# Kernel optimization log

Measured on AMD Instinct MI355X. Metric: run time of the kernel, lower is better.

The kernel has to match this reference:

```python
import jax, jax.numpy as jnp
import numpy as np

N = [80000, 70000, 50000]   # entities per type (flattened over the ragged batch)
F = [64, 128, 48]           # feature width per entity type
D = 512                     # d_model
B = 64                      # number of episodes in the ragged batch
EPS_IN = 1e-4               # InputNorm eps
EPS_LN = 1e-5               # LayerNorm eps
CLIP = 5.0                  # InputNorm cliprange


def setup_inputs() -> dict:
    key = jax.random.key(0)
    ks = jax.random.split(key, 3 * 7 + 2)
    inp = {}
    for i, (n, f) in enumerate(zip(N, F)):
        base = 7 * i
        inp[f"ent{i}"] = jax.random.normal(ks[base], (n, f), dtype=jnp.float32)
        inp[f"mean{i}"] = 0.1 * jax.random.normal(ks[base + 1], (f,), dtype=jnp.float32)
        inp[f"var{i}"] = jax.random.uniform(ks[base + 2], (f,), minval=0.5, maxval=1.5, dtype=jnp.float32)
        inp[f"W{i}"] = jax.random.normal(ks[base + 3], (f, D), dtype=jnp.float32) / np.sqrt(f)
        inp[f"b{i}"] = jnp.zeros((D,), dtype=jnp.float32)
        inp[f"gamma{i}"] = jnp.ones((D,), dtype=jnp.float32)
        inp[f"beta{i}"] = jnp.zeros((D,), dtype=jnp.float32)
    total = sum(N)
    # index_map: permutation reassembling per-type blocks into ragged episode order
    inp["index_map"] = jax.random.permutation(ks[-2], total).astype(jnp.int64)
    inp["batch_index"] = jnp.sort(jax.random.randint(ks[-1], (total,), 0, B)).astype(jnp.int64)
    return inp


def _embed(x, mean, var, W, b, gamma, beta):
    # InputNorm: normalize with running stats, clip outliers
    h = jnp.clip((x - mean) * jax.lax.rsqrt(var + EPS_IN), -CLIP, CLIP)
    # Linear + ReLU
    h = jnp.maximum(h @ W + b, 0.0)
    # LayerNorm
    mu = h.mean(-1, keepdims=True)
    v = ((h - mu) ** 2).mean(-1, keepdims=True)
    return gamma * (h - mu) * jax.lax.rsqrt(v + EPS_LN) + beta


def reference(ent0, mean0, var0, W0, b0, gamma0, beta0,
              ent1, mean1, var1, W1, b1, gamma1, beta1,
              ent2, mean2, var2, W2, b2, gamma2, beta2,
              index_map, batch_index):
    embeds = [
        _embed(ent0, mean0, var0, W0, b0, gamma0, beta0),
        _embed(ent1, mean1, var1, W1, b1, gamma1, beta1),
        _embed(ent2, mean2, var2, W2, b2, gamma2, beta2),
    ]
    x = jnp.concatenate(embeds, axis=0)                      # [sum(N), D]
    entity_type = jnp.concatenate(
        [jnp.full((n, 1), float(i), dtype=jnp.float32) for i, n in enumerate(N)], axis=0
    )
    # ragged reorder: gather-based reassembly into episode-major order
    x = x[index_map]
    entity_types = entity_type[index_map]
    tbatch_index = batch_index[index_map]
    return x, tbatch_index, entity_types
```

## Files before the change

kernel.cpp:

```cpp
#include <hip/hip_runtime.h>

#define DMODEL 512
#define EPS_IN 1e-4f
#define EPS_LN 1e-5f
#define CLIPV  5.0f

typedef float f32x4 __attribute__((ext_vector_type(4)));
typedef short s16x8 __attribute__((ext_vector_type(8)));

__device__ __forceinline__ unsigned short f2bf(float f) {
    union { float f; unsigned u; } v; v.f = f;
    unsigned r = v.u + 0x7fffu + ((v.u >> 16) & 1u);
    return (unsigned short)(r >> 16);
}

struct TypeParams {
    const float* x;
    const float* ss;
    const unsigned short* Wt;
    const float* b; const float* gamma; const float* beta;
    int n;
    int offset;
    int nb;
};

__global__ __launch_bounds__(256) void setup_all(
    const int* __restrict__ index_map, const int* __restrict__ batch_index,
    int* __restrict__ inv, float* __restrict__ out_t, float* __restrict__ out_e,
    int total, int n0, int n01, int nbA,
    const float* __restrict__ W0, const float* __restrict__ W1, const float* __restrict__ W2,
    unsigned short* __restrict__ Wt0, unsigned short* __restrict__ Wt1, unsigned short* __restrict__ Wt2,
    const float* __restrict__ mean0, const float* __restrict__ var0,
    const float* __restrict__ mean1, const float* __restrict__ var1,
    const float* __restrict__ mean2, const float* __restrict__ var2,
    float* __restrict__ ss0, float* __restrict__ ss1, float* __restrict__ ss2)
{
    const int nbB = (DMODEL * 256) / 256;
    if (blockIdx.x < (unsigned)nbA) {
        const int j = blockIdx.x * 256 + threadIdx.x;
        if (j >= total) return;
        const int r = index_map[j];
        inv[r] = j;
        out_t[j] = (float)batch_index[r];
        out_e[j] = (r < n0) ? 0.0f : ((r < n01) ? 1.0f : 2.0f);
    } else if (blockIdx.x < (unsigned)(nbA + nbB)) {
        int idx = (blockIdx.x - nbA) * 256 + threadIdx.x;
        const float* W; unsigned short* Wt; int K, Kp;
        if (idx < DMODEL * 64)              { W = W0; Wt = Wt0; K = 64;  Kp = 64; }
        else if (idx < DMODEL * (64 + 128)) { idx -= DMODEL * 64;  W = W1; Wt = Wt1; K = 128; Kp = 128; }
        else                                { idx -= DMODEL * 192; W = W2; Wt = Wt2; K = 48;  Kp = 64; }
        const int nn = idx / Kp, k = idx - nn * Kp;
        const float w = (k < K) ? W[(size_t)k * DMODEL + nn] : 0.0f;
        Wt[idx] = f2bf(w);
    } else {
        const int c = threadIdx.x;
        if (c < 64)  { const float s = rsqrtf(var0[c] + EPS_IN); ss0[c] = s; ss0[64 + c]  = -mean0[c] * s; }
        if (c < 128) { const float s = rsqrtf(var1[c] + EPS_IN); ss1[c] = s; ss1[128 + c] = -mean1[c] * s; }
        if (c < 48)  { const float s = rsqrtf(var2[c] + EPS_IN); ss2[c] = s; ss2[48 + c]  = -mean2[c] * s; }
    }
}

template<int F, int KP>
__device__ __forceinline__ void embed_body(
    const TypeParams& p, int bid, const int* __restrict__ inv,
    float* __restrict__ out, char* lds)
{
    const int tid  = threadIdx.x;
    const int lane = tid & 63;
    const int wn   = tid >> 6;
    const int l15  = lane & 15;
    const int g    = lane >> 4;
    const int row0 = bid * 32;
    const int n    = p.n;
    constexpr int SEG = KP / 8;
    constexpr int NKS = KP / 32;

    float2* red = reinterpret_cast<float2*>(lds + NKS * 2048);

    if (tid < 32 * SEG) {
        const int r = tid & 31;
        const int s = tid >> 5;
        const int gr = row0 + r;
        const int c = s * 8;
        s16x8 pk;
#pragma unroll
        for (int jj = 0; jj < 8; ++jj) pk[jj] = 0;
        if (gr < n && c < F) {
            const float4 x0 = *(const float4*)(p.x + (size_t)gr * F + c);
            const float4 x1 = *(const float4*)(p.x + (size_t)gr * F + c + 4);
            const float4 sc0 = *(const float4*)(p.ss + c);
            const float4 sc1 = *(const float4*)(p.ss + c + 4);
            const float4 sh0 = *(const float4*)(p.ss + F + c);
            const float4 sh1 = *(const float4*)(p.ss + F + c + 4);
            float t[8];
            t[0] = fmaf(x0.x, sc0.x, sh0.x); t[1] = fmaf(x0.y, sc0.y, sh0.y);
            t[2] = fmaf(x0.z, sc0.z, sh0.z); t[3] = fmaf(x0.w, sc0.w, sh0.w);
            t[4] = fmaf(x1.x, sc1.x, sh1.x); t[5] = fmaf(x1.y, sc1.y, sh1.y);
            t[6] = fmaf(x1.z, sc1.z, sh1.z); t[7] = fmaf(x1.w, sc1.w, sh1.w);
#pragma unroll
            for (int jj = 0; jj < 8; ++jj)
                pk[jj] = (short)f2bf(fminf(fmaxf(t[jj], -CLIPV), CLIPV));
        }
        *reinterpret_cast<s16x8*>(lds + tid * 16) = pk;
    }
    __syncthreads();

    int orow[2];
#pragma unroll
    for (int m = 0; m < 2; ++m) {
        const int rg = row0 + m * 16 + l15;
        orow[m] = (rg < n) ? inv[p.offset + rg] : -1;
    }

    f32x4 acc[2][4];
#pragma unroll
    for (int m = 0; m < 2; ++m)
#pragma unroll
        for (int t = 0; t < 4; ++t) acc[m][t] = (f32x4)0.0f;

    const unsigned short* wtl = p.Wt + (size_t)(wn * 64 + l15) * KP + g * 8;

#pragma unroll
    for (int ks = 0; ks < NKS; ++ks) {
        const int ab = ((ks * 4 + g) * 32 + l15) * 16;
        const s16x8 a0 = *reinterpret_cast<const s16x8*>(lds + ab);
        const s16x8 a1 = *reinterpret_cast<const s16x8*>(lds + ab + 256);
#pragma unroll
        for (int t = 0; t < 4; ++t) {
            const s16x8 wf = *reinterpret_cast<const s16x8*>(wtl + (size_t)t * 16 * KP + ks * 32);
            acc[0][t] = __builtin_amdgcn_mfma_f32_16x16x32_bf16(wf, a0, acc[0][t], 0, 0, 0);
            acc[1][t] = __builtin_amdgcn_mfma_f32_16x16x32_bf16(wf, a1, acc[1][t], 0, 0, 0);
        }
    }

#pragma unroll
    for (int t = 0; t < 4; ++t) {
        const float4 bb = *(const float4*)(p.b + wn * 64 + t * 16 + g * 4);
#pragma unroll
        for (int m = 0; m < 2; ++m) {
            acc[m][t][0] = fmaxf(acc[m][t][0] + bb.x, 0.0f);
            acc[m][t][1] = fmaxf(acc[m][t][1] + bb.y, 0.0f);
            acc[m][t][2] = fmaxf(acc[m][t][2] + bb.z, 0.0f);
            acc[m][t][3] = fmaxf(acc[m][t][3] + bb.w, 0.0f);
        }
    }

    {
        float ps[2] = {0.0f, 0.0f}, pq[2] = {0.0f, 0.0f};
#pragma unroll
        for (int m = 0; m < 2; ++m)
#pragma unroll
            for (int t = 0; t < 4; ++t)
#pragma unroll
                for (int j = 0; j < 4; ++j) {
                    const float v = acc[m][t][j];
                    ps[m] += v;
                    pq[m] = fmaf(v, v, pq[m]);
                }
#pragma unroll
        for (int m = 0; m < 2; ++m) {
            ps[m] += __shfl_xor(ps[m], 16, 64);
            pq[m] += __shfl_xor(pq[m], 16, 64);
            ps[m] += __shfl_xor(ps[m], 32, 64);
            pq[m] += __shfl_xor(pq[m], 32, 64);
        }
        if (g == 0) {
#pragma unroll
            for (int m = 0; m < 2; ++m)
                red[(m * 16 + l15) * 8 + wn] = make_float2(ps[m], pq[m]);
        }
    }
    __syncthreads();

#pragma unroll
    for (int m = 0; m < 2; ++m) {
        const int od = orow[m];
        if (od < 0) continue;
        const int rl = m * 16 + l15;
        float s = 0.0f, q = 0.0f;
#pragma unroll
        for (int wq = 0; wq < 8; ++wq) { const float2 e = red[rl * 8 + wq]; s += e.x; q += e.y; }
        const float mu = s * (1.0f / DMODEL);
        const float vv = fmaxf(q * (1.0f / DMODEL) - mu * mu, 0.0f);
        const float sc = rsqrtf(vv + EPS_LN);
        float* op = out + (size_t)od * DMODEL + wn * 64 + g * 4;
#pragma unroll
        for (int t = 0; t < 4; ++t) {
            const float4 gg = *(const float4*)(p.gamma + wn * 64 + t * 16 + g * 4);
            const float4 ee = *(const float4*)(p.beta  + wn * 64 + t * 16 + g * 4);
            float4 o;
            o.x = fmaf(gg.x * sc, acc[m][t][0] - mu, ee.x);
            o.y = fmaf(gg.y * sc, acc[m][t][1] - mu, ee.y);
            o.z = fmaf(gg.z * sc, acc[m][t][2] - mu, ee.z);
            o.w = fmaf(gg.w * sc, acc[m][t][3] - mu, ee.w);
            *(float4*)(op + t * 16) = o;
        }
    }
}

__global__ __launch_bounds__(512, 6) void embed_all(
    TypeParams p0, TypeParams p1, TypeParams p2,
    const int* __restrict__ inv, float* __restrict__ out)
{
    extern __shared__ char lds[];
    const int bid = blockIdx.x;
    if (bid < p0.nb)                embed_body<64, 64>  (p0, bid, inv, out, lds);
    else if (bid < p0.nb + p1.nb)   embed_body<128, 128>(p1, bid - p0.nb, inv, out, lds);
    else                            embed_body<48, 64>  (p2, bid - p0.nb - p1.nb, inv, out, lds);
}

extern "C" void kernel_launch(void* const* d_in, const int* in_sizes, int n_in,
                              void* d_out, int out_size, void* d_ws, size_t ws_size,
                              hipStream_t stream)
{
    const int F0 = 64, F1 = 128, F2 = 48;
    const int n0 = in_sizes[0]  / F0;
    const int n1 = in_sizes[7]  / F1;
    const int n2 = in_sizes[14] / F2;
    const int total = n0 + n1 + n2;

    float* out   = (float*)d_out;
    float* out_t = out + (size_t)total * DMODEL;
    float* out_e = out_t + total;

    int* inv = (int*)d_ws;
    unsigned short* Wt0 = (unsigned short*)((char*)d_ws + (((size_t)total * 4 + 255) & ~(size_t)255));
    unsigned short* Wt1 = Wt0 + DMODEL * 64;
    unsigned short* Wt2 = Wt1 + DMODEL * 128;
    float* ss0 = (float*)(Wt2 + DMODEL * 64);
    float* ss1 = ss0 + 128;
    float* ss2 = ss1 + 256;

    const int* index_map   = (const int*)d_in[21];
    const int* batch_index = (const int*)d_in[22];

    const int nbA = (total + 255) / 256;
    const int nbB = (DMODEL * 256) / 256;
    setup_all<<<nbA + nbB + 1, 256, 0, stream>>>(
        index_map, batch_index, inv, out_t, out_e, total, n0, n0 + n1, nbA,
        (const float*)d_in[3], (const float*)d_in[10], (const float*)d_in[17],
        Wt0, Wt1, Wt2,
        (const float*)d_in[1],  (const float*)d_in[2],
        (const float*)d_in[8],  (const float*)d_in[9],
        (const float*)d_in[15], (const float*)d_in[16],
        ss0, ss1, ss2);

    TypeParams p0{(const float*)d_in[0],  ss0, Wt0,
                  (const float*)d_in[4],  (const float*)d_in[5],  (const float*)d_in[6],
                  n0, 0,       (n0 + 31) / 32};
    TypeParams p1{(const float*)d_in[7],  ss1, Wt1,
                  (const float*)d_in[11], (const float*)d_in[12], (const float*)d_in[13],
                  n1, n0,      (n1 + 31) / 32};
    TypeParams p2{(const float*)d_in[14], ss2, Wt2,
                  (const float*)d_in[18], (const float*)d_in[19], (const float*)d_in[20],
                  n2, n0 + n1, (n2 + 31) / 32};

    const int nb = p0.nb + p1.nb + p2.nb;
    const int lds_size = 4 * 2048 + 32 * 8 * sizeof(float2);
    embed_all<<<nb, 512, lds_size, stream>>>(p0, p1, p2, inv, out);
}
```

Measured before the change: 185.8 us.

## Make embed blocks persistent over tiles with double-buffered prefetch of next tile

Each block now processes about four 32-row tiles in a strided loop instead of one. The next tile's input rows and inverse indices are loaded into registers during the current tile's MFMA and LayerNorm work, and staging alternates between two LDS buffers. Per-type scale/shift vectors are hoisted out of the loop. This adds registers and LDS per block and lowers the occupancy hint from 6 to 4 waves, with fewer blocks to spread across CUs.

```diff
diff --git a/kernel.cpp b/kernel.cpp
--- a/kernel.cpp
+++ b/kernel.cpp
@@ -65,140 +65,177 @@
     const TypeParams& p, int bid, const int* __restrict__ inv,
     float* __restrict__ out, char* lds)
 {
+    constexpr int SEG    = KP / 8;
+    constexpr int ABYTES = 32 * KP * 2;
+    constexpr int NKS    = KP / 32;
     const int tid  = threadIdx.x;
     const int lane = tid & 63;
     const int wn   = tid >> 6;
     const int l15  = lane & 15;
     const int g    = lane >> 4;
-    const int row0 = bid * 32;
     const int n    = p.n;
-    constexpr int SEG = KP / 8;
-    constexpr int NKS = KP / 32;
-
-    float2* red = reinterpret_cast<float2*>(lds + NKS * 2048);
-
-    if (tid < 32 * SEG) {
-        const int r = tid & 31;
-        const int s = tid >> 5;
-        const int gr = row0 + r;
-        const int c = s * 8;
+    const int NB   = p.nb;
+    const int ntiles = (n + 31) >> 5;
+
+    float2* red = reinterpret_cast<float2*>(lds + 2 * ABYTES);
+
+    const bool stg  = tid < 32 * SEG;
+    const int  sr   = tid & 31;
+    const int  scol = (tid >> 5) * 8;
+
+    float4 sA0 = {0,0,0,0}, sA1 = {0,0,0,0}, sB0 = {0,0,0,0}, sB1 = {0,0,0,0};
+    if (stg && scol < F) {
+        sA0 = *(const float4*)(p.ss + scol);
+        sA1 = *(const float4*)(p.ss + scol + 4);
+        sB0 = *(const float4*)(p.ss + F + scol);
+        sB1 = *(const float4*)(p.ss + F + scol + 4);
+    }
+
+    auto loadx = [&](int t, float4& x0, float4& x1) {
+        x0 = float4{0,0,0,0}; x1 = x0;
+        const int row = t * 32 + sr;
+        if (stg && row < n && scol < F) {
+            x0 = *(const float4*)(p.x + (size_t)row * F + scol);
+            x1 = *(const float4*)(p.x + (size_t)row * F + scol + 4);
+        }
+    };
+    auto loadinv = [&](int t, int* o) {
+#pragma unroll
+        for (int m = 0; m < 2; ++m) {
+            const int rg = t * 32 + m * 16 + l15;
+            o[m] = (rg < n) ? inv[p.offset + rg] : -1;
+        }
+    };
+    auto transform = [&](const float4& x0, const float4& x1) -> s16x8 {
+        float tv[8];
+        tv[0] = fmaf(x0.x, sA0.x, sB0.x); tv[1] = fmaf(x0.y, sA0.y, sB0.y);
+        tv[2] = fmaf(x0.z, sA0.z, sB0.z); tv[3] = fmaf(x0.w, sA0.w, sB0.w);
+        tv[4] = fmaf(x1.x, sA1.x, sB1.x); tv[5] = fmaf(x1.y, sA1.y, sB1.y);
+        tv[6] = fmaf(x1.z, sA1.z, sB1.z); tv[7] = fmaf(x1.w, sA1.w, sB1.w);
         s16x8 pk;
 #pragma unroll
-        for (int jj = 0; jj < 8; ++jj) pk[jj] = 0;
-        if (gr < n && c < F) {
-            const float4 x0 = *(const float4*)(p.x + (size_t)gr * F + c);
-            const float4 x1 = *(const float4*)(p.x + (size_t)gr * F + c + 4);
-            const float4 sc0 = *(const float4*)(p.ss + c);
-            const float4 sc1 = *(const float4*)(p.ss + c + 4);
-            const float4 sh0 = *(const float4*)(p.ss + F + c);
-            const float4 sh1 = *(const float4*)(p.ss + F + c + 4);
-            float t[8];
-            t[0] = fmaf(x0.x, sc0.x, sh0.x); t[1] = fmaf(x0.y, sc0.y, sh0.y);
-            t[2] = fmaf(x0.z, sc0.z, sh0.z); t[3] = fmaf(x0.w, sc0.w, sh0.w);
-            t[4] = fmaf(x1.x, sc1.x, sh1.x); t[5] = fmaf(x1.y, sc1.y, sh1.y);
-            t[6] = fmaf(x1.z, sc1.z, sh1.z); t[7] = fmaf(x1.w, sc1.w, sh1.w);
-#pragma unroll
-            for (int jj = 0; jj < 8; ++jj)
-                pk[jj] = (short)f2bf(fminf(fmaxf(t[jj], -CLIPV), CLIPV));
-        }
-        *reinterpret_cast<s16x8*>(lds + tid * 16) = pk;
+        for (int jj = 0; jj < 8; ++jj)
+            pk[jj] = (short)f2bf(fminf(fmaxf(tv[jj], -CLIPV), CLIPV));
+        return pk;
+    };
+
+    int tile = bid;
+    if (tile >= ntiles) return;
+    s16x8 pk;
+    int corow[2];
+    {
+        float4 x0, x1;
+        loadx(tile, x0, x1);
+        loadinv(tile, corow);
+        pk = transform(x0, x1);
     }
-    __syncthreads();
-
-    int orow[2];
-#pragma unroll
-    for (int m = 0; m < 2; ++m) {
-        const int rg = row0 + m * 16 + l15;
-        orow[m] = (rg < n) ? inv[p.offset + rg] : -1;
+    int pipe = 0;
+
+    const unsigned short* wtl = p.Wt + (size_t)(wn * 64 + l15) * KP + g * 8;
+
+    while (tile < ntiles) {
+        const int next = tile + NB;
+        const bool hn = next < ntiles;
+
+        if (stg) *reinterpret_cast<s16x8*>(lds + pipe * ABYTES + tid * 16) = pk;
+        __syncthreads();
+
+        float4 nx0 = {0,0,0,0}, nx1 = {0,0,0,0};
+        int norow[2] = {-1, -1};
+        if (hn) { loadx(next, nx0, nx1); loadinv(next, norow); }
+
+        f32x4 acc[2][4];
+#pragma unroll
+        for (int m = 0; m < 2; ++m)
+#pragma unroll
+            for (int t = 0; t < 4; ++t) acc[m][t] = (f32x4)0.0f;
+
+        const char* ab = lds + pipe * ABYTES;
+#pragma unroll
+        for (int ks = 0; ks < NKS; ++ks) {
+            const int off = ((ks * 4 + g) * 32 + l15) * 16;
+            const s16x8 a0 = *reinterpret_cast<const s16x8*>(ab + off);
+            const s16x8 a1 = *reinterpret_cast<const s16x8*>(ab + off + 256);
+#pragma unroll
+            for (int t = 0; t < 4; ++t) {
+                const s16x8 wf = *reinterpret_cast<const s16x8*>(wtl + (size_t)t * 16 * KP + ks * 32);
+                acc[0][t] = __builtin_amdgcn_mfma_f32_16x16x32_bf16(wf, a0, acc[0][t], 0, 0, 0);
+                acc[1][t] = __builtin_amdgcn_mfma_f32_16x16x32_bf16(wf, a1, acc[1][t], 0, 0, 0);
+            }
+        }
+
+#pragma unroll
+        for (int t = 0; t < 4; ++t) {
+            const float4 bb = *(const float4*)(p.b + wn * 64 + t * 16 + g * 4);
+#pragma unroll
+            for (int m = 0; m < 2; ++m) {
+                acc[m][t][0] = fmaxf(acc[m][t][0] + bb.x, 0.0f);
+                acc[m][t][1] = fmaxf(acc[m][t][1] + bb.y, 0.0f);
+                acc[m][t][2] = fmaxf(acc[m][t][2] + bb.z, 0.0f);
+                acc[m][t][3] = fmaxf(acc[m][t][3] + bb.w, 0.0f);
+            }
+        }
+
+        {
+            float ps[2] = {0.0f, 0.0f}, pq[2] = {0.0f, 0.0f};
+#pragma unroll
+            for (int m = 0; m < 2; ++m)
+#pragma unroll
+                for (int t = 0; t < 4; ++t)
+#pragma unroll
+                    for (int j = 0; j < 4; ++j) {
+                        const float v = acc[m][t][j];
+                        ps[m] += v;
+                        pq[m] = fmaf(v, v, pq[m]);
+                    }
+#pragma unroll
+            for (int m = 0; m < 2; ++m) {
+                ps[m] += __shfl_xor(ps[m], 16, 64);
+                pq[m] += __shfl_xor(pq[m], 16, 64);
+                ps[m] += __shfl_xor(ps[m], 32, 64);
+                pq[m] += __shfl_xor(pq[m], 32, 64);
+            }
+            if (g == 0) {
+#pragma unroll
+                for (int m = 0; m < 2; ++m)
+                    red[(m * 16 + l15) * 8 + wn] = make_float2(ps[m], pq[m]);
+            }
+        }
+        __syncthreads();
+
+#pragma unroll
+        for (int m = 0; m < 2; ++m) {
+            const int od = corow[m];
+            if (od < 0) continue;
+            const int rl = m * 16 + l15;
+            float s = 0.0f, q = 0.0f;
+#pragma unroll
+            for (int wq = 0; wq < 8; ++wq) { const float2 e = red[rl * 8 + wq]; s += e.x; q += e.y; }
+            const float mu = s * (1.0f / DMODEL);
+            const float vv = fmaxf(q * (1.0f / DMODEL) - mu * mu, 0.0f);
+            const float sc = rsqrtf(vv + EPS_LN);
+            float* op = out + (size_t)od * DMODEL + wn * 64 + g * 4;
+#pragma unroll
+            for (int t = 0; t < 4; ++t) {
+                const float4 gg = *(const float4*)(p.gamma + wn * 64 + t * 16 + g * 4);
+                const float4 ee = *(const float4*)(p.beta  + wn * 64 + t * 16 + g * 4);
+                float4 o;
+                o.x = fmaf(gg.x * sc, acc[m][t][0] - mu, ee.x);
+                o.y = fmaf(gg.y * sc, acc[m][t][1] - mu, ee.y);
+                o.z = fmaf(gg.z * sc, acc[m][t][2] - mu, ee.z);
+                o.w = fmaf(gg.w * sc, acc[m][t][3] - mu, ee.w);
+                *(float4*)(op + t * 16) = o;
+            }
+        }
+
+        pk = transform(nx0, nx1);
+        corow[0] = norow[0]; corow[1] = norow[1];
+        pipe ^= 1;
+        tile = next;
     }
-
-    f32x4 acc[2][4];
-#pragma unroll
-    for (int m = 0; m < 2; ++m)
-#pragma unroll
-        for (int t = 0; t < 4; ++t) acc[m][t] = (f32x4)0.0f;
-
-    const unsigned short* wtl = p.Wt + (size_t)(wn * 64 + l15) * KP + g * 8;
-
-#pragma unroll
-    for (int ks = 0; ks < NKS; ++ks) {
-        const int ab = ((ks * 4 + g) * 32 + l15) * 16;
-        const s16x8 a0 = *reinterpret_cast<const s16x8*>(lds + ab);
-        const s16x8 a1 = *reinterpret_cast<const s16x8*>(lds + ab + 256);
-#pragma unroll
-        for (int t = 0; t < 4; ++t) {
-            const s16x8 wf = *reinterpret_cast<const s16x8*>(wtl + (size_t)t * 16 * KP + ks * 32);
-            acc[0][t] = __builtin_amdgcn_mfma_f32_16x16x32_bf16(wf, a0, acc[0][t], 0, 0, 0);
-            acc[1][t] = __builtin_amdgcn_mfma_f32_16x16x32_bf16(wf, a1, acc[1][t], 0, 0, 0);
-        }
-    }
-
-#pragma unroll
-    for (int t = 0; t < 4; ++t) {
-        const float4 bb = *(const float4*)(p.b + wn * 64 + t * 16 + g * 4);
-#pragma unroll
-        for (int m = 0; m < 2; ++m) {
-            acc[m][t][0] = fmaxf(acc[m][t][0] + bb.x, 0.0f);
-            acc[m][t][1] = fmaxf(acc[m][t][1] + bb.y, 0.0f);
-            acc[m][t][2] = fmaxf(acc[m][t][2] + bb.z, 0.0f);
-            acc[m][t][3] = fmaxf(acc[m][t][3] + bb.w, 0.0f);
-        }
-    }
-
-    {
-        float ps[2] = {0.0f, 0.0f}, pq[2] = {0.0f, 0.0f};
-#pragma unroll
-        for (int m = 0; m < 2; ++m)
-#pragma unroll
-            for (int t = 0; t < 4; ++t)
-#pragma unroll
-                for (int j = 0; j < 4; ++j) {
-                    const float v = acc[m][t][j];
-                    ps[m] += v;
-                    pq[m] = fmaf(v, v, pq[m]);
-                }
-#pragma unroll
-        for (int m = 0; m < 2; ++m) {
-            ps[m] += __shfl_xor(ps[m], 16, 64);
-            pq[m] += __shfl_xor(pq[m], 16, 64);
-            ps[m] += __shfl_xor(ps[m], 32, 64);
-            pq[m] += __shfl_xor(pq[m], 32, 64);
-        }
-        if (g == 0) {
-#pragma unroll
-            for (int m = 0; m < 2; ++m)
-                red[(m * 16 + l15) * 8 + wn] = make_float2(ps[m], pq[m]);
-        }
-    }
-    __syncthreads();
-
-#pragma unroll
-    for (int m = 0; m < 2; ++m) {
-        const int od = orow[m];
-        if (od < 0) continue;
-        const int rl = m * 16 + l15;
-        float s = 0.0f, q = 0.0f;
-#pragma unroll
-        for (int wq = 0; wq < 8; ++wq) { const float2 e = red[rl * 8 + wq]; s += e.x; q += e.y; }
-        const float mu = s * (1.0f / DMODEL);
-        const float vv = fmaxf(q * (1.0f / DMODEL) - mu * mu, 0.0f);
-        const float sc = rsqrtf(vv + EPS_LN);
-        float* op = out + (size_t)od * DMODEL + wn * 64 + g * 4;
-#pragma unroll
-        for (int t = 0; t < 4; ++t) {
-            const float4 gg = *(const float4*)(p.gamma + wn * 64 + t * 16 + g * 4);
-            const float4 ee = *(const float4*)(p.beta  + wn * 64 + t * 16 + g * 4);
-            float4 o;
-            o.x = fmaf(gg.x * sc, acc[m][t][0] - mu, ee.x);
-            o.y = fmaf(gg.y * sc, acc[m][t][1] - mu, ee.y);
-            o.z = fmaf(gg.z * sc, acc[m][t][2] - mu, ee.z);
-            o.w = fmaf(gg.w * sc, acc[m][t][3] - mu, ee.w);
-            *(float4*)(op + t * 16) = o;
-        }
-    }
-}
-
-__global__ __launch_bounds__(512, 6) void embed_all(
+}
+
+__global__ __launch_bounds__(512, 4) void embed_all(
     TypeParams p0, TypeParams p1, TypeParams p2,
     const int* __restrict__ inv, float* __restrict__ out)
 {
@@ -218,6 +255,7 @@
     const int n1 = in_sizes[7]  / F1;
     const int n2 = in_sizes[14] / F2;
     const int total = n0 + n1 + n2;
+    const int TPB = 4;
 
     float* out   = (float*)d_out;
     float* out_t = out + (size_t)total * DMODEL;
@@ -245,17 +283,22 @@
         (const float*)d_in[15], (const float*)d_in[16],
         ss0, ss1, ss2);
 
+    const int nt0 = (n0 + 31) / 32, nt1 = (n1 + 31) / 32, nt2 = (n2 + 31) / 32;
+    const int NB0 = (nt0 + TPB - 1) / TPB;
+    const int NB1 = (nt1 + TPB - 1) / TPB;
+    const int NB2 = (nt2 + TPB - 1) / TPB;
+
     TypeParams p0{(const float*)d_in[0],  ss0, Wt0,
                   (const float*)d_in[4],  (const float*)d_in[5],  (const float*)d_in[6],
-                  n0, 0,       (n0 + 31) / 32};
+                  n0, 0,       NB0};
     TypeParams p1{(const float*)d_in[7],  ss1, Wt1,
                   (const float*)d_in[11], (const float*)d_in[12], (const float*)d_in[13],
-                  n1, n0,      (n1 + 31) / 32};
+                  n1, n0,      NB1};
     TypeParams p2{(const float*)d_in[14], ss2, Wt2,
                   (const float*)d_in[18], (const float*)d_in[19], (const float*)d_in[20],
-                  n2, n0 + n1, (n2 + 31) / 32};
-
-    const int nb = p0.nb + p1.nb + p2.nb;
-    const int lds_size = 4 * 2048 + 32 * 8 * sizeof(float2);
+                  n2, n0 + n1, NB2};
+
+    const int nb = NB0 + NB1 + NB2;
+    const int lds_size = 2 * (32 * 128 * 2) + 32 * 8 * sizeof(float2);
     embed_all<<<nb, 512, lds_size, stream>>>(p0, p1, p2, inv, out);
 }
```

New measurement: 218.7 us. 17.7% more time.

## Retile embed kernel to 16-row tiles with 4 waves covering 128 columns each

Applied to the files above, without the earlier changes.

Each block now handles 16 rows with 256 threads, and each wave computes 128 output columns (8 MFMA tiles) instead of 32 rows with 8 waves of 64 columns. This shrinks LDS use and the cross-wave LayerNorm reduction and doubles the block count. In exchange, each loaded weight fragment is reused for only one A tile instead of two, so weight traffic per row rises, and the launch bounds change to 256 threads with 5 blocks per CU.

```diff
diff --git a/kernel.cpp b/kernel.cpp
--- a/kernel.cpp
+++ b/kernel.cpp
@@ -62,36 +62,35 @@
 
 template<int F, int KP>
 __device__ __forceinline__ void embed_body(
-    const TypeParams& p, int bid, const int* __restrict__ inv,
+    const TypeParams& p, int tile, const int* __restrict__ inv,
     float* __restrict__ out, char* lds)
 {
+    constexpr int SEG = KP / 8;
+    constexpr int NKS = KP / 32;
     const int tid  = threadIdx.x;
     const int lane = tid & 63;
     const int wn   = tid >> 6;
     const int l15  = lane & 15;
     const int g    = lane >> 4;
-    const int row0 = bid * 32;
+    const int row0 = tile * 16;
     const int n    = p.n;
-    constexpr int SEG = KP / 8;
-    constexpr int NKS = KP / 32;
-
-    float2* red = reinterpret_cast<float2*>(lds + NKS * 2048);
-
-    if (tid < 32 * SEG) {
-        const int r = tid & 31;
-        const int s = tid >> 5;
+
+    float2* red = reinterpret_cast<float2*>(lds + 16 * KP * 2);
+
+    if (tid < 16 * SEG) {
+        const int r = tid & 15;
+        const int scol = (tid >> 4) * 8;
         const int gr = row0 + r;
-        const int c = s * 8;
         s16x8 pk;
 #pragma unroll
         for (int jj = 0; jj < 8; ++jj) pk[jj] = 0;
-        if (gr < n && c < F) {
-            const float4 x0 = *(const float4*)(p.x + (size_t)gr * F + c);
-            const float4 x1 = *(const float4*)(p.x + (size_t)gr * F + c + 4);
-            const float4 sc0 = *(const float4*)(p.ss + c);
-            const float4 sc1 = *(const float4*)(p.ss + c + 4);
-            const float4 sh0 = *(const float4*)(p.ss + F + c);
-            const float4 sh1 = *(const float4*)(p.ss + F + c + 4);
+        if (gr < n && scol < F) {
+            const float4 x0 = *(const float4*)(p.x + (size_t)gr * F + scol);
+            const float4 x1 = *(const float4*)(p.x + (size_t)gr * F + scol + 4);
+            const float4 sc0 = *(const float4*)(p.ss + scol);
+            const float4 sc1 = *(const float4*)(p.ss + scol + 4);
+            const float4 sh0 = *(const float4*)(p.ss + F + scol);
+            const float4 sh1 = *(const float4*)(p.ss + F + scol + 4);
             float t[8];
             t[0] = fmaf(x0.x, sc0.x, sh0.x); t[1] = fmaf(x0.y, sc0.y, sh0.y);
             t[2] = fmaf(x0.z, sc0.z, sh0.z); t[3] = fmaf(x0.w, sc0.w, sh0.w);
@@ -105,100 +104,75 @@
     }
     __syncthreads();
 
-    int orow[2];
-#pragma unroll
-    for (int m = 0; m < 2; ++m) {
-        const int rg = row0 + m * 16 + l15;
-        orow[m] = (rg < n) ? inv[p.offset + rg] : -1;
-    }
-
-    f32x4 acc[2][4];
-#pragma unroll
-    for (int m = 0; m < 2; ++m)
-#pragma unroll
-        for (int t = 0; t < 4; ++t) acc[m][t] = (f32x4)0.0f;
-
-    const unsigned short* wtl = p.Wt + (size_t)(wn * 64 + l15) * KP + g * 8;
+    const int rg = row0 + l15;
+    const int od = (rg < n) ? inv[p.offset + rg] : -1;
+
+    f32x4 acc[8];
+#pragma unroll
+    for (int t = 0; t < 8; ++t) acc[t] = (f32x4)0.0f;
+
+    const unsigned short* wtl = p.Wt + (size_t)(wn * 128 + l15) * KP + g * 8;
 
 #pragma unroll
     for (int ks = 0; ks < NKS; ++ks) {
-        const int ab = ((ks * 4 + g) * 32 + l15) * 16;
-        const s16x8 a0 = *reinterpret_cast<const s16x8*>(lds + ab);
-        const s16x8 a1 = *reinterpret_cast<const s16x8*>(lds + ab + 256);
-#pragma unroll
-        for (int t = 0; t < 4; ++t) {
+        const s16x8 a = *reinterpret_cast<const s16x8*>(lds + (ks * 4 + g) * 256 + l15 * 16);
+#pragma unroll
+        for (int t = 0; t < 8; ++t) {
             const s16x8 wf = *reinterpret_cast<const s16x8*>(wtl + (size_t)t * 16 * KP + ks * 32);
-            acc[0][t] = __builtin_amdgcn_mfma_f32_16x16x32_bf16(wf, a0, acc[0][t], 0, 0, 0);
-            acc[1][t] = __builtin_amdgcn_mfma_f32_16x16x32_bf16(wf, a1, acc[1][t], 0, 0, 0);
+            acc[t] = __builtin_amdgcn_mfma_f32_16x16x32_bf16(wf, a, acc[t], 0, 0, 0);
         }
     }
 
 #pragma unroll
-    for (int t = 0; t < 4; ++t) {
-        const float4 bb = *(const float4*)(p.b + wn * 64 + t * 16 + g * 4);
-#pragma unroll
-        for (int m = 0; m < 2; ++m) {
-            acc[m][t][0] = fmaxf(acc[m][t][0] + bb.x, 0.0f);
-            acc[m][t][1] = fmaxf(acc[m][t][1] + bb.y, 0.0f);
-            acc[m][t][2] = fmaxf(acc[m][t][2] + bb.z, 0.0f);
-            acc[m][t][3] = fmaxf(acc[m][t][3] + bb.w, 0.0f);
-        }
+    for (int t = 0; t < 8; ++t) {
+        const float4 bb = *(const float4*)(p.b + wn * 128 + t * 16 + g * 4);
+        acc[t][0] = fmaxf(acc[t][0] + bb.x, 0.0f);
+        acc[t][1] = fmaxf(acc[t][1] + bb.y, 0.0f);
+        acc[t][2] = fmaxf(acc[t][2] + bb.z, 0.0f);
+        acc[t][3] = fmaxf(acc[t][3] + bb.w, 0.0f);
     }
 
     {
-        float ps[2] = {0.0f, 0.0f}, pq[2] = {0.0f, 0.0f};
-#pragma unroll
-        for (int m = 0; m < 2; ++m)
-#pragma unroll
-            for (int t = 0; t < 4; ++t)
-#pragma unroll
-                for (int j = 0; j < 4; ++j) {
-                    const float v = acc[m][t][j];
-                    ps[m] += v;
-                    pq[m] = fmaf(v, v, pq[m]);
-                }
-#pragma unroll
-        for (int m = 0; m < 2; ++m) {
-            ps[m] += __shfl_xor(ps[m], 16, 64);
-            pq[m] += __shfl_xor(pq[m], 16, 64);
-            ps[m] += __shfl_xor(ps[m], 32, 64);
-            pq[m] += __shfl_xor(pq[m], 32, 64);
-        }
-        if (g == 0) {
-#pragma unroll
-            for (int m = 0; m < 2; ++m)
-                red[(m * 16 + l15) * 8 + wn] = make_float2(ps[m], pq[m]);
-        }
+        float ps = 0.0f, pq = 0.0f;
+#pragma unroll
+        for (int t = 0; t < 8; ++t)
+#pragma unroll
+            for (int j = 0; j < 4; ++j) {
+                const float v = acc[t][j];
+                ps += v;
+                pq = fmaf(v, v, pq);
+            }
+        ps += __shfl_xor(ps, 16, 64);
+        pq += __shfl_xor(pq, 16, 64);
+        ps += __shfl_xor(ps, 32, 64);
+        pq += __shfl_xor(pq, 32, 64);
+        if (g == 0) red[l15 * 4 + wn] = make_float2(ps, pq);
     }
     __syncthreads();
 
-#pragma unroll
-    for (int m = 0; m < 2; ++m) {
-        const int od = orow[m];
-        if (od < 0) continue;
-        const int rl = m * 16 + l15;
+    if (od >= 0) {
         float s = 0.0f, q = 0.0f;
 #pragma unroll
-        for (int wq = 0; wq < 8; ++wq) { const float2 e = red[rl * 8 + wq]; s += e.x; q += e.y; }
+        for (int wq = 0; wq < 4; ++wq) { const float2 e = red[l15 * 4 + wq]; s += e.x; q += e.y; }
         const float mu = s * (1.0f / DMODEL);
         const float vv = fmaxf(q * (1.0f / DMODEL) - mu * mu, 0.0f);
         const float sc = rsqrtf(vv + EPS_LN);
-        float* op = out + (size_t)od * DMODEL + wn * 64 + g * 4;
-#pragma unroll
-        for (int t = 0; t < 4; ++t) {
-            const float4 gg = *(const float4*)(p.gamma + wn * 64 + t * 16 + g * 4);
-            const float4 ee = *(const float4*)(p.beta  + wn * 64 + t * 16 + g * 4);
+        float* op = out + (size_t)od * DMODEL + wn * 128 + g * 4;
+#pragma unroll
+        for (int t = 0; t < 8; ++t) {
+            const float4 gg = *(const float4*)(p.gamma + wn * 128 + t * 16 + g * 4);
+            const float4 ee = *(const float4*)(p.beta  + wn * 128 + t * 16 + g * 4);
             float4 o;
-            o.x = fmaf(gg.x * sc, acc[m][t][0] - mu, ee.x);
-            o.y = fmaf(gg.y * sc, acc[m][t][1] - mu, ee.y);
-            o.z = fmaf(gg.z * sc, acc[m][t][2] - mu, ee.z);
-            o.w = fmaf(gg.w * sc, acc[m][t][3] - mu, ee.w);
+            o.x = fmaf(gg.x * sc, acc[t][0] - mu, ee.x);
+            o.y = fmaf(gg.y * sc, acc[t][1] - mu, ee.y);
+            o.z = fmaf(gg.z * sc, acc[t][2] - mu, ee.z);
+            o.w = fmaf(gg.w * sc, acc[t][3] - mu, ee.w);
             *(float4*)(op + t * 16) = o;
         }
     }
 }
 
-__global__ __launch_bounds__(512, 6) void embed_all(
+__global__ __launch_bounds__(256, 5) void embed_all(
     TypeParams p0, TypeParams p1, TypeParams p2,
     const int* __restrict__ inv, float* __restrict__ out)
 {
@@ -247,15 +221,15 @@
 
     TypeParams p0{(const float*)d_in[0],  ss0, Wt0,
                   (const float*)d_in[4],  (const float*)d_in[5],  (const float*)d_in[6],
-                  n0, 0,       (n0 + 31) / 32};
+                  n0, 0,       (n0 + 15) / 16};
     TypeParams p1{(const float*)d_in[7],  ss1, Wt1,
                   (const float*)d_in[11], (const float*)d_in[12], (const float*)d_in[13],
-                  n1, n0,      (n1 + 31) / 32};
+                  n1, n0,      (n1 + 15) / 16};
     TypeParams p2{(const float*)d_in[14], ss2, Wt2,
                   (const float*)d_in[18], (const float*)d_in[19], (const float*)d_in[20],
-                  n2, n0 + n1, (n2 + 31) / 32};
+                  n2, n0 + n1, (n2 + 15) / 16};
 
     const int nb = p0.nb + p1.nb + p2.nb;
-    const int lds_size = 4 * 2048 + 32 * 8 * sizeof(float2);
-    embed_all<<<nb, 512, lds_size, stream>>>(p0, p1, p2, inv, out);
-}
+    const int lds_size = 16 * 128 * 2 + 16 * 4 * sizeof(float2);
+    embed_all<<<nb, 256, lds_size, stream>>>(p0, p1, p2, inv, out);
+}
```

New measurement: 240.7 us. 29.5% more time.

## Pre-pack normalized bf16 activations in MFMA tile layout and load via direct-to-LDS

Applied to the files above, without the earlier changes.

Moves the InputNorm + clip + bf16 conversion of the entity features out of the embed kernel into the setup kernel, writing each 32-row tile in the exact LDS fragment layout. The embed kernel then fills LDS with global_load_lds 16-byte copies instead of doing fp32 loads, math and LDS stores, and drops the separate scale/shift precompute. This adds an extra workspace round-trip for the packed bf16 activations, which is half the fp32 size, and keeps the old path as a fallback when the workspace is too small. Occupancy hints also change: 5 for the new kernel, 4 for the fallback.

```diff
diff --git a/kernel.cpp b/kernel.cpp
--- a/kernel.cpp
+++ b/kernel.cpp
@@ -14,17 +14,233 @@
     return (unsigned short)(r >> 16);
 }
 
-struct TypeParams {
-    const float* x;
-    const float* ss;
+__device__ __forceinline__ void gload16(const void* g, void* l) {
+    __builtin_amdgcn_global_load_lds(
+        (const __attribute__((address_space(1))) unsigned int*)g,
+        (__attribute__((address_space(3))) unsigned int*)l, 16, 0, 0);
+}
+
+
+struct PackArgs {
+    const float* x; const float* mean; const float* var;
+    char* Ap;
+    int n, F, SEG, KP, nblocks;
+};
+
+__device__ __forceinline__ void pack_tile(const PackArgs& q, int lb) {
+    const int idx = lb * 256 + threadIdx.x;
+    int s, rg;
+    if (q.SEG == 8) { s = idx & 7;  rg = idx >> 3; }
+    else            { s = idx & 15; rg = idx >> 4; }
+    const int c = s * 8;
+    s16x8 pk;
+#pragma unroll
+    for (int j = 0; j < 8; ++j) pk[j] = 0;
+    if (rg < q.n && c < q.F) {
+        const float4 x0 = *(const float4*)(q.x + (size_t)rg * q.F + c);
+        const float4 x1 = *(const float4*)(q.x + (size_t)rg * q.F + c + 4);
+        const float4 m0 = *(const float4*)(q.mean + c);
+        const float4 m1 = *(const float4*)(q.mean + c + 4);
+        const float4 v0 = *(const float4*)(q.var + c);
+        const float4 v1 = *(const float4*)(q.var + c + 4);
+        float t[8];
+        t[0] = (x0.x - m0.x) * rsqrtf(v0.x + EPS_IN);
+        t[1] = (x0.y - m0.y) * rsqrtf(v0.y + EPS_IN);
+        t[2] = (x0.z - m0.z) * rsqrtf(v0.z + EPS_IN);
+        t[3] = (x0.w - m0.w) * rsqrtf(v0.w + EPS_IN);
+        t[4] = (x1.x - m1.x) * rsqrtf(v1.x + EPS_IN);
+        t[5] = (x1.y - m1.y) * rsqrtf(v1.y + EPS_IN);
+        t[6] = (x1.z - m1.z) * rsqrtf(v1.z + EPS_IN);
+        t[7] = (x1.w - m1.w) * rsqrtf(v1.w + EPS_IN);
+#pragma unroll
+        for (int j = 0; j < 8; ++j)
+            pk[j] = (short)f2bf(fminf(fmaxf(t[j], -CLIPV), CLIPV));
+    }
+    const int r = rg & 31, tile = rg >> 5;
+    const int off = (s >> 2) * 2048 + ((r >> 4) << 10) + (((s & 3) * 16 + (r & 15)) << 4);
+    *(s16x8*)(q.Ap + (size_t)tile * (q.KP * 64) + off) = pk;
+}
+
+__global__ __launch_bounds__(256) void prep_packed(
+    const int* __restrict__ index_map, const int* __restrict__ batch_index,
+    int* __restrict__ inv, float* __restrict__ out_t, float* __restrict__ out_e,
+    int total, int n0, int n01, int nbA,
+    const float* __restrict__ W0, const float* __restrict__ W1, const float* __restrict__ W2,
+    unsigned short* __restrict__ Wt0, unsigned short* __restrict__ Wt1, unsigned short* __restrict__ Wt2,
+    PackArgs q0, PackArgs q1, PackArgs q2)
+{
+    int b = blockIdx.x;
+    if (b < nbA) {
+        const int j = b * 256 + threadIdx.x;
+        if (j >= total) return;
+        const int r = index_map[j];
+        inv[r] = j;
+        out_t[j] = (float)batch_index[r];
+        out_e[j] = (r < n0) ? 0.0f : ((r < n01) ? 1.0f : 2.0f);
+        return;
+    }
+    b -= nbA;
+    if (b < 512) {
+        int idx = b * 256 + threadIdx.x;
+        const float* W; unsigned short* Wt; int K, Kp;
+        if (idx < DMODEL * 64)              { W = W0; Wt = Wt0; K = 64;  Kp = 64; }
+        else if (idx < DMODEL * (64 + 128)) { idx -= DMODEL * 64;  W = W1; Wt = Wt1; K = 128; Kp = 128; }
+        else                                { idx -= DMODEL * 192; W = W2; Wt = Wt2; K = 48;  Kp = 64; }
+        const int nn = idx / Kp, k = idx - nn * Kp;
+        const float w = (k < K) ? W[(size_t)k * DMODEL + nn] : 0.0f;
+        Wt[idx] = f2bf(w);
+        return;
+    }
+    b -= 512;
+    if (b < q0.nblocks) { pack_tile(q0, b); return; }
+    b -= q0.nblocks;
+    if (b < q1.nblocks) { pack_tile(q1, b); return; }
+    b -= q1.nblocks;
+    pack_tile(q2, b);
+}
+
+struct TypeParamsP {
+    const char* Ap;
     const unsigned short* Wt;
     const float* b; const float* gamma; const float* beta;
-    int n;
-    int offset;
-    int nb;
+    int n, offset, nb;
 };
 
-__global__ __launch_bounds__(256) void setup_all(
+template<int KP>
+__device__ __forceinline__ void embed_body_p(
+    const TypeParamsP& p, int tile, const int* __restrict__ inv,
+    float* __restrict__ out, char* lds)
+{
+    constexpr int NKS = KP / 32;
+    constexpr int TB  = KP * 64;
+    const int tid  = threadIdx.x;
+    const int lane = tid & 63;
+    const int wn   = tid >> 6;
+    const int l15  = lane & 15;
+    const int g    = lane >> 4;
+    const int n    = p.n;
+
+    float2* red = reinterpret_cast<float2*>(lds + 8192);
+
+    const char* src = p.Ap + (size_t)tile * TB;
+    if (KP == 128) {
+        gload16(src + tid * 16, lds + (tid >> 6) * 1024);
+    } else {
+        if (tid < 256) gload16(src + tid * 16, lds + (tid >> 6) * 1024);
+    }
+
+    int orow[2];
+#pragma unroll
+    for (int m = 0; m < 2; ++m) {
+        const int rg = tile * 32 + m * 16 + l15;
+        orow[m] = (rg < n) ? inv[p.offset + rg] : -1;
+    }
+    __syncthreads();
+
+    f32x4 acc[2][4];
+#pragma unroll
+    for (int m = 0; m < 2; ++m)
+#pragma unroll
+        for (int t = 0; t < 4; ++t) acc[m][t] = (f32x4)0.0f;
+
+    const unsigned short* wtl = p.Wt + (size_t)(wn * 64 + l15) * KP + g * 8;
+
+#pragma unroll
+    for (int ks = 0; ks < NKS; ++ks) {
+        const s16x8 a0 = *reinterpret_cast<const s16x8*>(lds + ks * 2048 + lane * 16);
+        const s16x8 a1 = *reinterpret_cast<const s16x8*>(lds + ks * 2048 + 1024 + lane * 16);
+#pragma unroll
+        for (int t = 0; t < 4; ++t) {
+            const s16x8 wf = *reinterpret_cast<const s16x8*>(wtl + (size_t)t * 16 * KP + ks * 32);
+            acc[0][t] = __builtin_amdgcn_mfma_f32_16x16x32_bf16(wf, a0, acc[0][t], 0, 0, 0);
+            acc[1][t] = __builtin_amdgcn_mfma_f32_16x16x32_bf16(wf, a1, acc[1][t], 0, 0, 0);
+        }
+    }
+
+#pragma unroll
+    for (int t = 0; t < 4; ++t) {
+        const float4 bb = *(const float4*)(p.b + wn * 64 + t * 16 + g * 4);
+#pragma unroll
+        for (int m = 0; m < 2; ++m) {
+            acc[m][t][0] = fmaxf(acc[m][t][0] + bb.x, 0.0f);
+            acc[m][t][1] = fmaxf(acc[m][t][1] + bb.y, 0.0f);
+            acc[m][t][2] = fmaxf(acc[m][t][2] + bb.z, 0.0f);
+            acc[m][t][3] = fmaxf(acc[m][t][3] + bb.w, 0.0f);
+        }
+    }
+
+    {
+        float ps[2] = {0.0f, 0.0f}, pq[2] = {0.0f, 0.0f};
+#pragma unroll
+        for (int m = 0; m < 2; ++m)
+#pragma unroll
+            for (int t = 0; t < 4; ++t)
+#pragma unroll
+                for (int j = 0; j < 4; ++j) {
+                    const float v = acc[m][t][j];
+                    ps[m] += v;
+                    pq[m] = fmaf(v, v, pq[m]);
+                }
+#pragma unroll
+        for (int m = 0; m < 2; ++m) {
+            ps[m] += __shfl_xor(ps[m], 16, 64);
+            pq[m] += __shfl_xor(pq[m], 16, 64);
+            ps[m] += __shfl_xor(ps[m], 32, 64);
+            pq[m] += __shfl_xor(pq[m], 32, 64);
+        }
+        if (g == 0) {
+#pragma unroll
+            for (int m = 0; m < 2; ++m)
+                red[(m * 16 + l15) * 8 + wn] = make_float2(ps[m], pq[m]);
+        }
+    }
+    __syncthreads();
+
+#pragma unroll
+    for (int m = 0; m < 2; ++m) {
+        const int od = orow[m];
+        if (od < 0) continue;
+        const int rl = m * 16 + l15;
+        float s = 0.0f, q = 0.0f;
+#pragma unroll
+        for (int wq = 0; wq < 8; ++wq) { const float2 e = red[rl * 8 + wq]; s += e.x; q += e.y; }
+        const float mu = s * (1.0f / DMODEL);
+        const float vv = fmaxf(q * (1.0f / DMODEL) - mu * mu, 0.0f);
+        const float sc = rsqrtf(vv + EPS_LN);
+        float* op = out + (size_t)od * DMODEL + wn * 64 + g * 4;
+#pragma unroll
+        for (int t = 0; t < 4; ++t) {
+            const float4 gg = *(const float4*)(p.gamma + wn * 64 + t * 16 + g * 4);
+            const float4 ee = *(const float4*)(p.beta  + wn * 64 + t * 16 + g * 4);
+            float4 o;
+            o.x = fmaf(gg.x * sc, acc[m][t][0] - mu, ee.x);
+            o.y = fmaf(gg.y * sc, acc[m][t][1] - mu, ee.y);
+            o.z = fmaf(gg.z * sc, acc[m][t][2] - mu, ee.z);
+            o.w = fmaf(gg.w * sc, acc[m][t][3] - mu, ee.w);
+            *(float4*)(op + t * 16) = o;
+        }
+    }
+}
+
+__global__ __launch_bounds__(512, 5) void embed_packed(
+    TypeParamsP p0, TypeParamsP p1, TypeParamsP p2,
+    const int* __restrict__ inv, float* __restrict__ out)
+{
+    __shared__ char lds[8192 + 32 * 8 * sizeof(float2)];
+    const int bid = blockIdx.x;
+    if (bid < p0.nb)                embed_body_p<64> (p0, bid, inv, out, lds);
+    else if (bid < p0.nb + p1.nb)   embed_body_p<128>(p1, bid - p0.nb, inv, out, lds);
+    else                            embed_body_p<64> (p2, bid - p0.nb - p1.nb, inv, out, lds);
+}
+
+
+struct TypeParams {
+    const float* x; const float* ss; const unsigned short* Wt;
+    const float* b; const float* gamma; const float* beta;
+    int n, offset, nb;
+};
+
+__global__ __launch_bounds__(256) void setup_fb(
     const int* __restrict__ index_map, const int* __restrict__ batch_index,
     int* __restrict__ inv, float* __restrict__ out_t, float* __restrict__ out_e,
     int total, int n0, int n01, int nbA,
@@ -35,7 +251,6 @@
     const float* __restrict__ mean2, const float* __restrict__ var2,
     float* __restrict__ ss0, float* __restrict__ ss1, float* __restrict__ ss2)
 {
-    const int nbB = (DMODEL * 256) / 256;
     if (blockIdx.x < (unsigned)nbA) {
         const int j = blockIdx.x * 256 + threadIdx.x;
         if (j >= total) return;
@@ -43,7 +258,7 @@
         inv[r] = j;
         out_t[j] = (float)batch_index[r];
         out_e[j] = (r < n0) ? 0.0f : ((r < n01) ? 1.0f : 2.0f);
-    } else if (blockIdx.x < (unsigned)(nbA + nbB)) {
+    } else if (blockIdx.x < (unsigned)(nbA + 512)) {
         int idx = (blockIdx.x - nbA) * 256 + threadIdx.x;
         const float* W; unsigned short* Wt; int K, Kp;
         if (idx < DMODEL * 64)              { W = W0; Wt = Wt0; K = 64;  Kp = 64; }
@@ -61,10 +276,12 @@
 }
 
 template<int F, int KP>
-__device__ __forceinline__ void embed_body(
+__device__ __forceinline__ void embed_body_fb(
     const TypeParams& p, int bid, const int* __restrict__ inv,
     float* __restrict__ out, char* lds)
 {
+    constexpr int SEG = KP / 8;
+    constexpr int NKS = KP / 32;
     const int tid  = threadIdx.x;
     const int lane = tid & 63;
     const int wn   = tid >> 6;
@@ -72,16 +289,14 @@
     const int g    = lane >> 4;
     const int row0 = bid * 32;
     const int n    = p.n;
-    constexpr int SEG = KP / 8;
-    constexpr int NKS = KP / 32;
 
     float2* red = reinterpret_cast<float2*>(lds + NKS * 2048);
 
     if (tid < 32 * SEG) {
         const int r = tid & 31;
         const int s = tid >> 5;
+        const int c = s * 8;
         const int gr = row0 + r;
-        const int c = s * 8;
         s16x8 pk;
 #pragma unroll
         for (int jj = 0; jj < 8; ++jj) pk[jj] = 0;
@@ -198,16 +413,17 @@
     }
 }
 
-__global__ __launch_bounds__(512, 6) void embed_all(
+__global__ __launch_bounds__(512, 4) void embed_fb(
     TypeParams p0, TypeParams p1, TypeParams p2,
     const int* __restrict__ inv, float* __restrict__ out)
 {
     extern __shared__ char lds[];
     const int bid = blockIdx.x;
-    if (bid < p0.nb)                embed_body<64, 64>  (p0, bid, inv, out, lds);
-    else if (bid < p0.nb + p1.nb)   embed_body<128, 128>(p1, bid - p0.nb, inv, out, lds);
-    else                            embed_body<48, 64>  (p2, bid - p0.nb - p1.nb, inv, out, lds);
-}
+    if (bid < p0.nb)                embed_body_fb<64, 64>  (p0, bid, inv, out, lds);
+    else if (bid < p0.nb + p1.nb)   embed_body_fb<128, 128>(p1, bid - p0.nb, inv, out, lds);
+    else                            embed_body_fb<48, 64>  (p2, bid - p0.nb - p1.nb, inv, out, lds);
+}
+
 
 extern "C" void kernel_launch(void* const* d_in, const int* in_sizes, int n_in,
                               void* d_out, int out_size, void* d_ws, size_t ws_size,
@@ -218,44 +434,73 @@
     const int n1 = in_sizes[7]  / F1;
     const int n2 = in_sizes[14] / F2;
     const int total = n0 + n1 + n2;
+    const int nt0 = (n0 + 31) / 32, nt1 = (n1 + 31) / 32, nt2 = (n2 + 31) / 32;
 
     float* out   = (float*)d_out;
     float* out_t = out + (size_t)total * DMODEL;
     float* out_e = out_t + total;
 
     int* inv = (int*)d_ws;
-    unsigned short* Wt0 = (unsigned short*)((char*)d_ws + (((size_t)total * 4 + 255) & ~(size_t)255));
+    size_t off = (((size_t)total * 4) + 255) & ~(size_t)255;
+    unsigned short* Wt0 = (unsigned short*)((char*)d_ws + off);
     unsigned short* Wt1 = Wt0 + DMODEL * 64;
     unsigned short* Wt2 = Wt1 + DMODEL * 128;
     float* ss0 = (float*)(Wt2 + DMODEL * 64);
     float* ss1 = ss0 + 128;
     float* ss2 = ss1 + 256;
+    size_t aoff = ((off + (size_t)DMODEL * 256 * 2 + 4096) + 255) & ~(size_t)255;
+    char* A0 = (char*)d_ws + aoff;
+    char* A1 = A0 + (size_t)nt0 * 4096;
+    char* A2 = A1 + (size_t)nt1 * 8192;
+    const size_t need = aoff + (size_t)nt0 * 4096 + (size_t)nt1 * 8192 + (size_t)nt2 * 4096;
 
     const int* index_map   = (const int*)d_in[21];
     const int* batch_index = (const int*)d_in[22];
-
     const int nbA = (total + 255) / 256;
-    const int nbB = (DMODEL * 256) / 256;
-    setup_all<<<nbA + nbB + 1, 256, 0, stream>>>(
-        index_map, batch_index, inv, out_t, out_e, total, n0, n0 + n1, nbA,
-        (const float*)d_in[3], (const float*)d_in[10], (const float*)d_in[17],
-        Wt0, Wt1, Wt2,
-        (const float*)d_in[1],  (const float*)d_in[2],
-        (const float*)d_in[8],  (const float*)d_in[9],
-        (const float*)d_in[15], (const float*)d_in[16],
-        ss0, ss1, ss2);
-
-    TypeParams p0{(const float*)d_in[0],  ss0, Wt0,
-                  (const float*)d_in[4],  (const float*)d_in[5],  (const float*)d_in[6],
-                  n0, 0,       (n0 + 31) / 32};
-    TypeParams p1{(const float*)d_in[7],  ss1, Wt1,
-                  (const float*)d_in[11], (const float*)d_in[12], (const float*)d_in[13],
-                  n1, n0,      (n1 + 31) / 32};
-    TypeParams p2{(const float*)d_in[14], ss2, Wt2,
-                  (const float*)d_in[18], (const float*)d_in[19], (const float*)d_in[20],
-                  n2, n0 + n1, (n2 + 31) / 32};
-
-    const int nb = p0.nb + p1.nb + p2.nb;
-    const int lds_size = 4 * 2048 + 32 * 8 * sizeof(float2);
-    embed_all<<<nb, 512, lds_size, stream>>>(p0, p1, p2, inv, out);
-}
+
+    if (ws_size >= need) {
+        PackArgs q0{(const float*)d_in[0],  (const float*)d_in[1],  (const float*)d_in[2],
+                    A0, n0, F0, 8,  64,  nt0};
+        PackArgs q1{(const float*)d_in[7],  (const float*)d_in[8],  (const float*)d_in[9],
+                    A1, n1, F1, 16, 128, nt1 * 2};
+        PackArgs q2{(const float*)d_in[14], (const float*)d_in[15], (const float*)d_in[16],
+                    A2, n2, F2, 8,  64,  nt2};
+
+        const int nbP = nbA + 512 + q0.nblocks + q1.nblocks + q2.nblocks;
+        prep_packed<<<nbP, 256, 0, stream>>>(
+            index_map, batch_index, inv, out_t, out_e, total, n0, n0 + n1, nbA,
+            (const float*)d_in[3], (const float*)d_in[10], (const float*)d_in[17],
+            Wt0, Wt1, Wt2, q0, q1, q2);
+
+        TypeParamsP p0{A0, Wt0, (const float*)d_in[4],  (const float*)d_in[5],  (const float*)d_in[6],
+                       n0, 0,       nt0};
+        TypeParamsP p1{A1, Wt1, (const float*)d_in[11], (const float*)d_in[12], (const float*)d_in[13],
+                       n1, n0,      nt1};
+        TypeParamsP p2{A2, Wt2, (const float*)d_in[18], (const float*)d_in[19], (const float*)d_in[20],
+                       n2, n0 + n1, nt2};
+
+        embed_packed<<<nt0 + nt1 + nt2, 512, 0, stream>>>(p0, p1, p2, inv, out);
+    } else {
+        setup_fb<<<nbA + 512 + 1, 256, 0, stream>>>(
+            index_map, batch_index, inv, out_t, out_e, total, n0, n0 + n1, nbA,
+            (const float*)d_in[3], (const float*)d_in[10], (const float*)d_in[17],
+            Wt0, Wt1, Wt2,
+            (const float*)d_in[1],  (const float*)d_in[2],
+            (const float*)d_in[8],  (const float*)d_in[9],
+            (const float*)d_in[15], (const float*)d_in[16],
+            ss0, ss1, ss2);
+
+        TypeParams p0{(const float*)d_in[0],  ss0, Wt0,
+                      (const float*)d_in[4],  (const float*)d_in[5],  (const float*)d_in[6],
+                      n0, 0,       nt0};
+        TypeParams p1{(const float*)d_in[7],  ss1, Wt1,
+                      (const float*)d_in[11], (const float*)d_in[12], (const float*)d_in[13],
+                      n1, n0,      nt1};
+        TypeParams p2{(const float*)d_in[14], ss2, Wt2,
+                      (const float*)d_in[18], (const float*)d_in[19], (const float*)d_in[20],
+                      n2, n0 + n1, nt2};
+
+        const int lds_size = 4 * 2048 + 32 * 8 * sizeof(float2);
+        embed_fb<<<nt0 + nt1 + nt2, 512, lds_size, stream>>>(p0, p1, p2, inv, out);
+    }
+}
```

New measurement: 179.4 us. -3.5%, faster.
